# Optimization experiments

Hardware: AMD Instinct MI355X
Metric: run time of the kernel (lower is better)

The kernel has to match this reference:

```python
import jax, jax.numpy as jnp
import numpy as np


def setup_inputs() -> dict:
    key = jax.random.key(0)
    k1, k2 = jax.random.split(key)
    C, V, DEG = 256, 512, 6  # checks, variables, ~avg row degree (LDPC-sparse)
    H = (jax.random.uniform(k1, (C, V)) < DEG / V).astype(jnp.int32)
    llr = jax.random.normal(k2, (V,), dtype=jnp.float32) * 4.0  # LLR-scale values
    return {"llr": llr, "H": H, "max_iter": 2}


def reference(llr, H, max_iter):
    # Faithful translation of LDPCBeliefPropagation.forward, including its
    # sequential in-place update semantics (later node updates read earlier ones
    # within the same sweep).
    C, V = H.shape
    Hf = H.astype(jnp.float32)          # (C, V)
    Hb_T = (H == 1).T                   # (V, C) mask: Hb_T[v, j] = H[j, v]==1
    m_vtoc = jnp.ones((V, C), jnp.float32)
    m_ctov = jnp.zeros((C, V), jnp.float32)
    phi = lambda s: 2.0 * jnp.arctan(jnp.exp(0.5 * s))
    jidx = jnp.arange(V)

    for _ in range(max_iter):
        # --- variable->check pass: sequential over variable i ---
        # Original: m_vtoc[i, j] = sign(llr[i]) * prod_{v: H[j,v]==1} tanh(0.5*m_vtoc[v, j])
        # Step i writes row i; reads of column j see all rows < i already updated,
        # so we scan over i and recompute the masked column products each step.
        def p1(m, i):
            prod = jnp.prod(jnp.where(Hb_T, jnp.tanh(0.5 * m), 1.0), axis=0)  # (C,)
            return m.at[i].set(jnp.sign(llr[i]) * prod), None

        m_vtoc, _ = jax.lax.scan(p1, m_vtoc, jnp.arange(V))
        mv = m_vtoc

        # --- check->variable pass: sequential over check i ---
        # Original inner loop over j writes m_ctov[i, j] and reads column i of
        # m_ctov. Within fixed i, the only written element that is re-read is
        # (i, i) (written at j == i), so for j > i the sum gets the exact
        # correction H[i, j] * (v_new - old (i,i)). Bit-exact to the nested loop.
        def p2(m, i):
            col = m[:, i]                                  # (C,) old column i
            base = col @ Hf - mv[:, i]                     # (V,) masked sum - m_vtoc[j, i]
            v_new = phi(base[i])                           # value written at j == i
            adj = jnp.where(jidx > i, Hf[i] * (v_new - col[i]), 0.0)
            return m.at[i].set(phi(base + adj)), None

        m_ctov, _ = jax.lax.scan(p2, m_ctov, jnp.arange(C))

    soft = jnp.sign(llr) * jnp.prod(jnp.tanh(0.5 * m_ctov), axis=0)  # (V,)
    return jnp.where(soft > 0, 1, 0).astype(jnp.int32)[0:4]  # hardcoded [0:4] as in source
```

## Files before the change

### kernel.cpp

```cpp
#include <hip/hip_runtime.h>

#define CC 256
#define VV 512
#define MAXRD 26
#define MAXCD 18
#define PSTRIDE 27
#define RINGD 8
#define CLU 6

typedef __attribute__((address_space(1))) float gfloat;

__device__ __forceinline__ float sgnf(float x) {
    return (x > 0.f) ? 1.f : ((x < 0.f) ? -1.f : 0.f);
}
__device__ __forceinline__ float phi_f(float x) {
    return 2.0f * atanf(expf(0.5f * x));
}
__device__ __forceinline__ void lds_barrier() {
    asm volatile("s_waitcnt lgkmcnt(0)" ::: "memory");
    __builtin_amdgcn_sched_barrier(0);
    __builtin_amdgcn_s_barrier();
    __builtin_amdgcn_sched_barrier(0);
}

__global__ __launch_bounds__(256)
void ldpc_bp8(const float* __restrict__ llr_g, const int* __restrict__ H_g,
              const int* __restrict__ it_g, int* __restrict__ out_g,
              float* __restrict__ ws)
{
    __shared__ float              llr_s[VV];
    __shared__ unsigned int       rsign[CC];
    __shared__ unsigned int       rzero[CC];
    __shared__ unsigned short     rdeg_s[CC];
    __shared__ float              Pst[CC][PSTRIDE];
    __shared__ unsigned short     clistT[MAXCD][CC];
    __shared__ unsigned short     cdeg_s[CC];
    __shared__ float              colbuf[2][257];
    __shared__ float              ring[RINGD][CC];
    __shared__ unsigned long long rowmask[CC][4];
    __shared__ unsigned char      rowpre[CC][4];

    const int j  = threadIdx.x;
    const int wv = j >> 6, ln = j & 63;
    gfloat* __restrict__ mg = (gfloat*)ws;

    llr_s[j] = llr_g[j]; llr_s[j + CC] = llr_g[j + CC];
    __syncthreads();
    {   int d = 0; unsigned int sb = 0, zb = 0;
        const int4* hrow = (const int4*)(H_g + j * VV);
        for (int g = 0; g < VV / 4; ++g) {
            int4 h = hrow[g]; const int v = g * 4;
            if (h.x) { if (d < MAXRD) { float l = llr_s[v+0]; sb |= (l < 0.f) << d; zb |= (l == 0.f) << d; } ++d; }
            if (h.y) { if (d < MAXRD) { float l = llr_s[v+1]; sb |= (l < 0.f) << d; zb |= (l == 0.f) << d; } ++d; }
            if (h.z) { if (d < MAXRD) { float l = llr_s[v+2]; sb |= (l < 0.f) << d; zb |= (l == 0.f) << d; } ++d; }
            if (h.w) { if (d < MAXRD) { float l = llr_s[v+3]; sb |= (l < 0.f) << d; zb |= (l == 0.f) << d; } ++d; }
        }
        rdeg_s[j] = (unsigned short)(d < MAXRD ? d : MAXRD);
        rsign[j] = sb; rzero[j] = zb;
    }
    {   int d = 0;
        for (int c = 0; c < CC; ++c) {
            const int h = H_g[c * VV + j];
            const unsigned long long m = __ballot(h != 0);
            if (ln == 0) rowmask[c][wv] = m;
            if (h) { if (d < MAXCD) clistT[d][j] = (unsigned short)c; ++d; }
        }
        cdeg_s[j] = (unsigned short)(d < MAXCD ? d : MAXCD);
        for (int k = d; k < MAXCD; ++k) clistT[k][j] = 256;
    }
    colbuf[0][j] = 0.0f;
    if (j == 0) { colbuf[0][256] = 0.0f; colbuf[1][256] = 0.0f; }
    __syncthreads();
    {   const int p1 = __popcll(rowmask[j][0]);
        const int p2 = p1 + __popcll(rowmask[j][1]);
        const int p3 = p2 + __popcll(rowmask[j][2]);
        rowpre[j][0] = 0; rowpre[j][1] = (unsigned char)p1;
        rowpre[j][2] = (unsigned char)p2; rowpre[j][3] = (unsigned char)p3;
    }
    const int cl0 = clistT[0][j], cl1 = clistT[1][j], cl2 = clistT[2][j];
    const int cl3 = clistT[3][j], cl4 = clistT[4][j], cl5 = clistT[5][j];
    const int cd  = cdeg_s[j];
    __syncthreads();

    const int   max_iter = it_g[0];
    const int   total    = max_iter * CC;
    const float T05      = tanhf(0.5f);
    const float sgj      = sgnf(llr_s[j]);

    float sv_base = 0.f, sv_bi = 0.f, sv_cbs = 0.f;
    int   sv_hv = 0;
    float val_prev = 0.f, fprod = 1.0f;

    auto STEP = [&](int T, float& pf_issue, float& pf_use) {
        const int s  = T & 255;
        const int Tc = T + 1;
        const int X1 = Tc & 255;

        const float* cb = colbuf[T & 1];
        const float g0 = cb[cl0], g1 = cb[cl1], g2 = cb[cl2];
        const float g3 = cb[cl3], g4 = cb[cl4], g5 = cb[cl5];
        const unsigned long long rm = rowmask[s][wv];
        const int   p     = T - ((T - j) & 255);
        const float ringv = ring[p & (RINGD - 1)][X1];
        pf_issue = mg[((T + 4) & 255) * CC + j];

        if (T > 0) {
            float vnp;
            if (sv_hv) { float vnew = phi_f(sv_bi); vnp = phi_f(sv_base + (vnew - sv_cbs)); }
            else       vnp = phi_f(sv_base);
            val_prev = vnp;
            ring[(T - 1) & (RINGD - 1)][j] = vnp;
            mg[j * CC + ((T - 1) & 255)] = vnp;
            if (j < 4 && (T - 1) >= total - CC) fprod *= tanhf(0.5f * vnp);
        }

        if (s == 0) {
            const int pass = T >> 8;
            const int deg  = rdeg_s[j];
            const unsigned int sb = rsign[j], zb = rzero[j];
            float NP = 1.0f;
            for (int k = 0; k <= deg; ++k) {
                float P = NP;
                for (int idx = k; idx < deg; ++idx) {
                    float told;
                    if (pass == 0) told = T05;
                    else {
                        const float sg = ((zb >> idx) & 1u) ? 0.0f
                                       : (((sb >> idx) & 1u) ? -1.0f : 1.0f);
                        told = tanhf(0.5f * (sg * Pst[j][idx]));
                    }
                    P *= told;
                }
                Pst[j][k] = P;
                if (k < deg) {
                    const float sg = ((zb >> k) & 1u) ? 0.0f
                                   : (((sb >> k) & 1u) ? -1.0f : 1.0f);
                    NP *= tanhf(0.5f * (sg * P));
                }
            }
            lds_barrier();
        }

        if (Tc < total && p <= T - 2) {
            float v;
            if (p >= T - 8)    v = ringv;
            else if (p >= 0)   v = pf_use;
            else               v = 0.0f;
            colbuf[Tc & 1][j] = v;
        }

        const int  kj  = (int)rowpre[s][wv] + __popcll(rm & ((1ull << ln) - 1ull));
        const bool hit = (rm >> ln) & 1ull;
        float sum = 0.0f;
        sum += g0; sum += g1; sum += g2; sum += g3; sum += g4; sum += g5;
        for (int k = CLU; k < cd; ++k) sum += cb[clistT[k][j]];
        const float base = sum - sgj * Pst[s][kj];
        const bool hv = hit && (j > s);
        float bi = 0.f, cbs = 0.f;
        if (hv) {
            float bsum = 0.0f;
            bsum += cb[clistT[0][s]]; bsum += cb[clistT[1][s]];
            bsum += cb[clistT[2][s]]; bsum += cb[clistT[3][s]];
            bsum += cb[clistT[4][s]]; bsum += cb[clistT[5][s]];
            const int cds = cdeg_s[s];
            for (int k = CLU; k < cds; ++k) bsum += cb[clistT[k][s]];
            const int ki = (int)rowpre[s][s >> 6]
                         + __popcll(rowmask[s][s >> 6] & ((1ull << (s & 63)) - 1ull));
            bi  = bsum - sgnf(llr_s[s]) * Pst[s][ki];
            cbs = cb[s];
        }
        sv_base = base; sv_bi = bi; sv_cbs = cbs; sv_hv = hv ? 1 : 0;

        if (Tc < total && j == X1) {
            float vo;
            if (hv) { float vnew = phi_f(bi); vo = phi_f(base + (vnew - cbs)); }
            else    vo = phi_f(base);
            colbuf[Tc & 1][s] = vo;
            colbuf[Tc & 1][(T - 1) & 255] = val_prev;
        }

        lds_barrier();
    };

    float p0 = 0.f, p1r = 0.f, p2r = 0.f, p3r = 0.f;
    #pragma unroll 1
    for (int T4 = 0; T4 < total; T4 += 4) {
        STEP(T4 + 0, p0,  p1r);
        STEP(T4 + 1, p1r, p2r);
        STEP(T4 + 2, p2r, p3r);
        STEP(T4 + 3, p3r, p0);
    }

    {
        float vnp;
        if (sv_hv) { float vnew = phi_f(sv_bi); vnp = phi_f(sv_base + (vnew - sv_cbs)); }
        else       vnp = phi_f(sv_base);
        if (j < 4) {
            fprod *= tanhf(0.5f * vnp);
            const float soft = sgj * fprod;
            out_g[j] = (soft > 0.0f) ? 1 : 0;
        }
    }
}

extern "C" void kernel_launch(void* const* d_in, const int* in_sizes, int n_in,
                              void* d_out, int out_size, void* d_ws, size_t ws_size,
                              hipStream_t stream) {
    const float* llr = (const float*)d_in[0];
    const int*   H   = (const int*)d_in[1];
    const int*   mi  = (const int*)d_in[2];
    int*         out = (int*)d_out;
    float*       ws  = (float*)d_ws;
    hipLaunchKernelGGL(ldpc_bp8, dim3(1), dim3(256), 0, stream,
                       llr, H, mi, out, ws);
}
```

Before: 554.5 us.

## Process two check rows per barrier step with speculative diagonal value

Restructures the sequential check-to-variable sweep so each loop iteration handles two consecutive check rows (A and B) with one LDS barrier instead of two. Row B's dependency on row A's result is handled by having every thread recompute the single diagonal value that changes (dval) and substitute it wherever row s is referenced. The column buffers are doubled to hold two pending columns, and ring and prefetch logic is adapted. This aims to halve the barrier count on the serial critical path, at the cost of redundant per-thread arithmetic and more LDS reads per step.

```diff
diff --git a/kernel.cpp b/kernel.cpp
--- a/kernel.cpp
+++ b/kernel.cpp
@@ -5,7 +5,6 @@
 #define MAXRD 26
 #define MAXCD 18
 #define PSTRIDE 27
-#define RINGD 8
 #define CLU 6
 
 typedef __attribute__((address_space(1))) float gfloat;
@@ -24,7 +23,7 @@
 }
 
 __global__ __launch_bounds__(256)
-void ldpc_bp8(const float* __restrict__ llr_g, const int* __restrict__ H_g,
+void ldpc_bp9(const float* __restrict__ llr_g, const int* __restrict__ H_g,
               const int* __restrict__ it_g, int* __restrict__ out_g,
               float* __restrict__ ws)
 {
@@ -35,8 +34,8 @@
     __shared__ float              Pst[CC][PSTRIDE];
     __shared__ unsigned short     clistT[MAXCD][CC];
     __shared__ unsigned short     cdeg_s[CC];
-    __shared__ float              colbuf[2][257];
-    __shared__ float              ring[RINGD][CC];
+    __shared__ float              colbuf[2][2][257];
+    __shared__ float              ring[8][CC];
     __shared__ unsigned long long rowmask[CC][4];
     __shared__ unsigned char      rowpre[CC][4];
 
@@ -68,14 +67,19 @@
         cdeg_s[j] = (unsigned short)(d < MAXCD ? d : MAXCD);
         for (int k = d; k < MAXCD; ++k) clistT[k][j] = 256;
     }
-    colbuf[0][j] = 0.0f;
-    if (j == 0) { colbuf[0][256] = 0.0f; colbuf[1][256] = 0.0f; }
+    colbuf[0][0][j] = 0.f; colbuf[0][1][j] = 0.f;
+    colbuf[1][0][j] = 0.f; colbuf[1][1][j] = 0.f;
+    for (int r = 0; r < 8; ++r) ring[r][j] = 0.f;
+    if (j == 0) {
+        colbuf[0][0][256] = 0.f; colbuf[0][1][256] = 0.f;
+        colbuf[1][0][256] = 0.f; colbuf[1][1][256] = 0.f;
+    }
     __syncthreads();
-    {   const int p1 = __popcll(rowmask[j][0]);
-        const int p2 = p1 + __popcll(rowmask[j][1]);
-        const int p3 = p2 + __popcll(rowmask[j][2]);
-        rowpre[j][0] = 0; rowpre[j][1] = (unsigned char)p1;
-        rowpre[j][2] = (unsigned char)p2; rowpre[j][3] = (unsigned char)p3;
+    {   const int p1c = __popcll(rowmask[j][0]);
+        const int p2c = p1c + __popcll(rowmask[j][1]);
+        const int p3c = p2c + __popcll(rowmask[j][2]);
+        rowpre[j][0] = 0; rowpre[j][1] = (unsigned char)p1c;
+        rowpre[j][2] = (unsigned char)p2c; rowpre[j][3] = (unsigned char)p3c;
     }
     const int cl0 = clistT[0][j], cl1 = clistT[1][j], cl2 = clistT[2][j];
     const int cl3 = clistT[3][j], cl4 = clistT[4][j], cl5 = clistT[5][j];
@@ -87,35 +91,56 @@
     const float T05      = tanhf(0.5f);
     const float sgj      = sgnf(llr_s[j]);
 
-    float sv_base = 0.f, sv_bi = 0.f, sv_cbs = 0.f;
-    int   sv_hv = 0;
-    float val_prev = 0.f, fprod = 1.0f;
-
-    auto STEP = [&](int T, float& pf_issue, float& pf_use) {
-        const int s  = T & 255;
-        const int Tc = T + 1;
-        const int X1 = Tc & 255;
-
-        const float* cb = colbuf[T & 1];
-        const float g0 = cb[cl0], g1 = cb[cl1], g2 = cb[cl2];
-        const float g3 = cb[cl3], g4 = cb[cl4], g5 = cb[cl5];
-        const unsigned long long rm = rowmask[s][wv];
-        const int   p     = T - ((T - j) & 255);
-        const float ringv = ring[p & (RINGD - 1)][X1];
-        pf_issue = mg[((T + 4) & 255) * CC + j];
-
-        if (T > 0) {
-            float vnp;
-            if (sv_hv) { float vnew = phi_f(sv_bi); vnp = phi_f(sv_base + (vnew - sv_cbs)); }
-            else       vnp = phi_f(sv_base);
-            val_prev = vnp;
-            ring[(T - 1) & (RINGD - 1)][j] = vnp;
-            mg[j * CC + ((T - 1) & 255)] = vnp;
-            if (j < 4 && (T - 1) >= total - CC) fprod *= tanhf(0.5f * vnp);
+    float svA_base = 0.f, svA_bi = 0.f, svA_cbs = 0.f; int svA_hv = 0;
+    float svB_base = 0.f, svB_bi = 0.f, svB_cbs = 0.f; int svB_hv = 0;
+    float pfu0 = 0.f, pfu1 = 0.f;
+    float fprod = 1.0f;
+
+    #pragma unroll 1
+    for (int Ts = 0; Ts < total; Ts += 2) {
+        const int s   = Ts & 255;
+        const int X1v = s + 1;
+        const int X2v = (Ts + 2) & 255;
+        const int X3v = (Ts + 3) & 255;
+        const int pr  = (Ts >> 1) & 1;
+        const float* cbA = colbuf[pr][0];
+        const float* cbB = colbuf[pr][1];
+        float* nxA = colbuf[pr ^ 1][0];
+        float* nxB = colbuf[pr ^ 1][1];
+
+        const float gA0 = cbA[cl0], gA1 = cbA[cl1], gA2 = cbA[cl2];
+        const float gA3 = cbA[cl3], gA4 = cbA[cl4], gA5 = cbA[cl5];
+        const float gB0 = cbB[cl0], gB1 = cbB[cl1], gB2 = cbB[cl2];
+        const float gB3 = cbB[cl3], gB4 = cbB[cl4], gB5 = cbB[cl5];
+        const unsigned long long rmA = rowmask[s][wv];
+        const unsigned long long rmB = rowmask[X1v][wv];
+        const int p = (Ts + 1) - ((Ts + 1 - j) & 255);
+        const float ringvA = ring[p & 7][X2v];
+        const float ringvB = ring[p & 7][X3v];
+        const float pfi0 = mg[((Ts + 4) & 255) * CC + j];
+        const float pfi1 = mg[((Ts + 5) & 255) * CC + j];
+        const int dc0 = clistT[0][X1v], dc1 = clistT[1][X1v], dc2 = clistT[2][X1v];
+        const int dc3 = clistT[3][X1v], dc4 = clistT[4][X1v], dc5 = clistT[5][X1v];
+        const int cdd = cdeg_s[X1v];
+
+        float vnpA = 0.f, vnpB = 0.f;
+        if (Ts >= 2) {
+            if (svA_hv) { float vn = phi_f(svA_bi); vnpA = phi_f(svA_base + (vn - svA_cbs)); }
+            else        vnpA = phi_f(svA_base);
+            if (svB_hv) { float vn = phi_f(svB_bi); vnpB = phi_f(svB_base + (vn - svB_cbs)); }
+            else        vnpB = phi_f(svB_base);
+            ring[(Ts - 2) & 7][j] = vnpA;
+            ring[(Ts - 1) & 7][j] = vnpB;
+            mg[j * CC + ((Ts - 2) & 255)] = vnpA;
+            mg[j * CC + ((Ts - 1) & 255)] = vnpB;
+            if (j < 4) {
+                if (Ts - 2 >= total - CC) fprod *= tanhf(0.5f * vnpA);
+                if (Ts - 1 >= total - CC) fprod *= tanhf(0.5f * vnpB);
+            }
         }
 
         if (s == 0) {
-            const int pass = T >> 8;
+            const int pass = Ts >> 8;
             const int deg  = rdeg_s[j];
             const unsigned int sb = rsign[j], zb = rzero[j];
             float NP = 1.0f;
@@ -141,62 +166,114 @@
             lds_barrier();
         }
 
-        if (Tc < total && p <= T - 2) {
-            float v;
-            if (p >= T - 8)    v = ringv;
-            else if (p >= 0)   v = pf_use;
-            else               v = 0.0f;
-            colbuf[Tc & 1][j] = v;
-        }
-
-        const int  kj  = (int)rowpre[s][wv] + __popcll(rm & ((1ull << ln) - 1ull));
-        const bool hit = (rm >> ln) & 1ull;
-        float sum = 0.0f;
-        sum += g0; sum += g1; sum += g2; sum += g3; sum += g4; sum += g5;
-        for (int k = CLU; k < cd; ++k) sum += cb[clistT[k][j]];
-        const float base = sum - sgj * Pst[s][kj];
-        const bool hv = hit && (j > s);
-        float bi = 0.f, cbs = 0.f;
-        if (hv) {
+        float dsum = 0.0f;
+        dsum += cbA[dc0]; dsum += cbA[dc1]; dsum += cbA[dc2];
+        dsum += cbA[dc3]; dsum += cbA[dc4]; dsum += cbA[dc5];
+        for (int k = CLU; k < cdd; ++k) dsum += cbA[clistT[k][X1v]];
+        const int kjd = (int)rowpre[s][X1v >> 6]
+                      + __popcll(rowmask[s][X1v >> 6] & ((1ull << (X1v & 63)) - 1ull));
+        const float bX1 = dsum - sgnf(llr_s[X1v]) * Pst[s][kjd];
+        const bool diag_hit = (rowmask[s][X1v >> 6] >> (X1v & 63)) & 1ull;
+        float dval;
+        if (diag_hit) {
+            float bs_ = 0.0f;
+            const int cds = cdeg_s[s];
+            for (int k = 0; k < cds; ++k) bs_ += cbA[clistT[k][s]];
+            const int kis = (int)rowpre[s][s >> 6]
+                          + __popcll(rowmask[s][s >> 6] & ((1ull << (s & 63)) - 1ull));
+            const float bis = bs_ - sgnf(llr_s[s]) * Pst[s][kis];
+            dval = phi_f(bX1 + (phi_f(bis) - cbA[s]));
+        } else {
+            dval = phi_f(bX1);
+        }
+
+        const unsigned long long lanelt = (1ull << ln) - 1ull;
+        const int  kjA  = (int)rowpre[s][wv] + __popcll(rmA & lanelt);
+        const bool hitA = (rmA >> ln) & 1ull;
+        float sumA = 0.0f;
+        sumA += gA0; sumA += gA1; sumA += gA2; sumA += gA3; sumA += gA4; sumA += gA5;
+        for (int k = CLU; k < cd; ++k) sumA += cbA[clistT[k][j]];
+        const float baseA = sumA - sgj * Pst[s][kjA];
+        const bool hvA = hitA && (j > s);
+        float biA = 0.f, cbsA = 0.f;
+        if (hvA) {
             float bsum = 0.0f;
-            bsum += cb[clistT[0][s]]; bsum += cb[clistT[1][s]];
-            bsum += cb[clistT[2][s]]; bsum += cb[clistT[3][s]];
-            bsum += cb[clistT[4][s]]; bsum += cb[clistT[5][s]];
             const int cds = cdeg_s[s];
-            for (int k = CLU; k < cds; ++k) bsum += cb[clistT[k][s]];
-            const int ki = (int)rowpre[s][s >> 6]
-                         + __popcll(rowmask[s][s >> 6] & ((1ull << (s & 63)) - 1ull));
-            bi  = bsum - sgnf(llr_s[s]) * Pst[s][ki];
-            cbs = cb[s];
-        }
-        sv_base = base; sv_bi = bi; sv_cbs = cbs; sv_hv = hv ? 1 : 0;
-
-        if (Tc < total && j == X1) {
-            float vo;
-            if (hv) { float vnew = phi_f(bi); vo = phi_f(base + (vnew - cbs)); }
-            else    vo = phi_f(base);
-            colbuf[Tc & 1][s] = vo;
-            colbuf[Tc & 1][(T - 1) & 255] = val_prev;
-        }
+            for (int k = 0; k < cds; ++k) bsum += cbA[clistT[k][s]];
+            const int kis2 = (int)rowpre[s][s >> 6]
+                           + __popcll(rowmask[s][s >> 6] & ((1ull << (s & 63)) - 1ull));
+            biA  = bsum - sgnf(llr_s[s]) * Pst[s][kis2];
+            cbsA = cbA[s];
+        }
+
+        const int  kjB  = (int)rowpre[X1v][wv] + __popcll(rmB & lanelt);
+        const bool hitB = (rmB >> ln) & 1ull;
+        const float tB0 = (cl0 == s) ? dval : gB0;
+        const float tB1 = (cl1 == s) ? dval : gB1;
+        const float tB2 = (cl2 == s) ? dval : gB2;
+        const float tB3 = (cl3 == s) ? dval : gB3;
+        const float tB4 = (cl4 == s) ? dval : gB4;
+        const float tB5 = (cl5 == s) ? dval : gB5;
+        float sumB = 0.0f;
+        sumB += tB0; sumB += tB1; sumB += tB2; sumB += tB3; sumB += tB4; sumB += tB5;
+        for (int k = CLU; k < cd; ++k) {
+            const int ci = clistT[k][j];
+            sumB += (ci == s) ? dval : cbB[ci];
+        }
+        const float baseB = sumB - sgj * Pst[X1v][kjB];
+        const bool hvB = hitB && (j > X1v);
+        float biB = 0.f, cbsB = 0.f;
+        if (hvB) {
+            float bsum = 0.0f;
+            const int cdsB = cdeg_s[X1v];
+            for (int k = 0; k < cdsB; ++k) {
+                const int ci = clistT[k][X1v];
+                bsum += (ci == s) ? dval : cbB[ci];
+            }
+            const int kiB = (int)rowpre[X1v][X1v >> 6]
+                          + __popcll(rowmask[X1v][X1v >> 6] & ((1ull << (X1v & 63)) - 1ull));
+            biB  = bsum - sgnf(llr_s[X1v]) * Pst[X1v][kiB];
+            cbsB = cbB[X1v];
+        }
+
+        if (j == X2v || j == X3v) {
+            float voT, voT1;
+            if (hvA) voT  = phi_f(baseA + (phi_f(biA) - cbsA)); else voT  = phi_f(baseA);
+            if (hvB) voT1 = phi_f(baseB + (phi_f(biB) - cbsB)); else voT1 = phi_f(baseB);
+            float* nx = (j == X2v) ? nxA : nxB;
+            nx[s]   = voT;
+            nx[X1v] = voT1;
+            if (Ts >= 2) {
+                nx[(Ts - 1) & 255] = vnpB;
+                nx[(Ts - 2) & 255] = vnpA;
+            }
+        }
+
+        if (p <= Ts - 3) {
+            float vA, vB;
+            if (p < 0)           { vA = 0.0f;   vB = 0.0f;   }
+            else if (p >= Ts - 8){ vA = ringvA; vB = ringvB; }
+            else                 { vA = pfu0;   vB = pfu1;   }
+            nxA[j] = vA;
+            nxB[j] = vB;
+        }
+
+        svA_base = baseA; svA_bi = biA; svA_cbs = cbsA; svA_hv = hvA ? 1 : 0;
+        svB_base = baseB; svB_bi = biB; svB_cbs = cbsB; svB_hv = hvB ? 1 : 0;
+        pfu0 = pfi0; pfu1 = pfi1;
 
         lds_barrier();
-    };
-
-    float p0 = 0.f, p1r = 0.f, p2r = 0.f, p3r = 0.f;
-    #pragma unroll 1
-    for (int T4 = 0; T4 < total; T4 += 4) {
-        STEP(T4 + 0, p0,  p1r);
-        STEP(T4 + 1, p1r, p2r);
-        STEP(T4 + 2, p2r, p3r);
-        STEP(T4 + 3, p3r, p0);
     }
 
     {
-        float vnp;
-        if (sv_hv) { float vnew = phi_f(sv_bi); vnp = phi_f(sv_base + (vnew - sv_cbs)); }
-        else       vnp = phi_f(sv_base);
+        float vnpA, vnpB;
+        if (svA_hv) { float vn = phi_f(svA_bi); vnpA = phi_f(svA_base + (vn - svA_cbs)); }
+        else        vnpA = phi_f(svA_base);
+        if (svB_hv) { float vn = phi_f(svB_bi); vnpB = phi_f(svB_base + (vn - svB_cbs)); }
+        else        vnpB = phi_f(svB_base);
         if (j < 4) {
-            fprod *= tanhf(0.5f * vnp);
+            fprod *= tanhf(0.5f * vnpA);
+            fprod *= tanhf(0.5f * vnpB);
             const float soft = sgj * fprod;
             out_g[j] = (soft > 0.0f) ? 1 : 0;
         }
@@ -211,6 +288,6 @@
     const int*   mi  = (const int*)d_in[2];
     int*         out = (int*)d_out;
     float*       ws  = (float*)d_ws;
-    hipLaunchKernelGGL(ldpc_bp8, dim3(1), dim3(256), 0, stream,
+    hipLaunchKernelGGL(ldpc_bp9, dim3(1), dim3(256), 0, stream,
                        llr, H, mi, out, ws);
 }
```

New measurement: 682.2 us. +23.0%, slower.

## Halve block to 128 threads with two columns per thread to cheapen barriers

Applied to the files above, without the earlier changes.

Launches the single-block kernel with 128 threads instead of 256, so each thread handles two variable columns j and j+128. The sequential per-step loop then synchronises 2 wavefronts per barrier instead of 4, which should make the 512 barrier-bound steps cheaper. In exchange each thread does twice the LDS reads and phi evaluations per step, and the shared bsum computation is done once for both columns. It also zero-initialises the ring buffer.

```diff
diff --git a/kernel.cpp b/kernel.cpp
--- a/kernel.cpp
+++ b/kernel.cpp
@@ -5,8 +5,8 @@
 #define MAXRD 26
 #define MAXCD 18
 #define PSTRIDE 27
-#define RINGD 8
 #define CLU 6
+#define NT  128
 
 typedef __attribute__((address_space(1))) float gfloat;
 
@@ -23,10 +23,10 @@
     __builtin_amdgcn_sched_barrier(0);
 }
 
-__global__ __launch_bounds__(256)
-void ldpc_bp8(const float* __restrict__ llr_g, const int* __restrict__ H_g,
-              const int* __restrict__ it_g, int* __restrict__ out_g,
-              float* __restrict__ ws)
+__global__ __launch_bounds__(NT)
+void ldpc_bp10(const float* __restrict__ llr_g, const int* __restrict__ H_g,
+               const int* __restrict__ it_g, int* __restrict__ out_g,
+               float* __restrict__ ws)
 {
     __shared__ float              llr_s[VV];
     __shared__ unsigned int       rsign[CC];
@@ -36,18 +36,25 @@
     __shared__ unsigned short     clistT[MAXCD][CC];
     __shared__ unsigned short     cdeg_s[CC];
     __shared__ float              colbuf[2][257];
-    __shared__ float              ring[RINGD][CC];
+    __shared__ float              ring[8][CC];
     __shared__ unsigned long long rowmask[CC][4];
     __shared__ unsigned char      rowpre[CC][4];
 
-    const int j  = threadIdx.x;
-    const int wv = j >> 6, ln = j & 63;
+    const int tid = threadIdx.x;
+    const int j0  = tid, j1 = tid + NT;
+    const int wv  = tid >> 6, ln = tid & 63;
     gfloat* __restrict__ mg = (gfloat*)ws;
 
-    llr_s[j] = llr_g[j]; llr_s[j + CC] = llr_g[j + CC];
+    llr_s[tid]       = llr_g[tid];
+    llr_s[tid + 128] = llr_g[tid + 128];
+    llr_s[tid + 256] = llr_g[tid + 256];
+    llr_s[tid + 384] = llr_g[tid + 384];
     __syncthreads();
-    {   int d = 0; unsigned int sb = 0, zb = 0;
-        const int4* hrow = (const int4*)(H_g + j * VV);
+    #pragma unroll 1
+    for (int rr = 0; rr < 2; ++rr) {
+        const int c = tid + rr * NT;
+        int d = 0; unsigned int sb = 0, zb = 0;
+        const int4* hrow = (const int4*)(H_g + c * VV);
         for (int g = 0; g < VV / 4; ++g) {
             int4 h = hrow[g]; const int v = g * 4;
             if (h.x) { if (d < MAXRD) { float l = llr_s[v+0]; sb |= (l < 0.f) << d; zb |= (l == 0.f) << d; } ++d; }
@@ -55,150 +62,205 @@
             if (h.z) { if (d < MAXRD) { float l = llr_s[v+2]; sb |= (l < 0.f) << d; zb |= (l == 0.f) << d; } ++d; }
             if (h.w) { if (d < MAXRD) { float l = llr_s[v+3]; sb |= (l < 0.f) << d; zb |= (l == 0.f) << d; } ++d; }
         }
-        rdeg_s[j] = (unsigned short)(d < MAXRD ? d : MAXRD);
-        rsign[j] = sb; rzero[j] = zb;
-    }
-    {   int d = 0;
+        rdeg_s[c] = (unsigned short)(d < MAXRD ? d : MAXRD);
+        rsign[c] = sb; rzero[c] = zb;
+    }
+    {
+        int d0 = 0, d1 = 0;
         for (int c = 0; c < CC; ++c) {
-            const int h = H_g[c * VV + j];
-            const unsigned long long m = __ballot(h != 0);
-            if (ln == 0) rowmask[c][wv] = m;
-            if (h) { if (d < MAXCD) clistT[d][j] = (unsigned short)c; ++d; }
-        }
-        cdeg_s[j] = (unsigned short)(d < MAXCD ? d : MAXCD);
-        for (int k = d; k < MAXCD; ++k) clistT[k][j] = 256;
-    }
-    colbuf[0][j] = 0.0f;
-    if (j == 0) { colbuf[0][256] = 0.0f; colbuf[1][256] = 0.0f; }
+            const int h0 = H_g[c * VV + j0];
+            const int h1 = H_g[c * VV + j1];
+            const unsigned long long m0 = __ballot(h0 != 0);
+            const unsigned long long m1 = __ballot(h1 != 0);
+            if (ln == 0) { rowmask[c][wv] = m0; rowmask[c][2 + wv] = m1; }
+            if (h0) { if (d0 < MAXCD) clistT[d0][j0] = (unsigned short)c; ++d0; }
+            if (h1) { if (d1 < MAXCD) clistT[d1][j1] = (unsigned short)c; ++d1; }
+        }
+        cdeg_s[j0] = (unsigned short)(d0 < MAXCD ? d0 : MAXCD);
+        cdeg_s[j1] = (unsigned short)(d1 < MAXCD ? d1 : MAXCD);
+        for (int k = d0; k < MAXCD; ++k) clistT[k][j0] = 256;
+        for (int k = d1; k < MAXCD; ++k) clistT[k][j1] = 256;
+    }
+    colbuf[0][j0] = 0.0f; colbuf[0][j1] = 0.0f;
+    #pragma unroll
+    for (int r = 0; r < 8; ++r) { ring[r][j0] = 0.0f; ring[r][j1] = 0.0f; }
+    if (tid == 0) { colbuf[0][256] = 0.0f; colbuf[1][256] = 0.0f; }
     __syncthreads();
-    {   const int p1 = __popcll(rowmask[j][0]);
-        const int p2 = p1 + __popcll(rowmask[j][1]);
-        const int p3 = p2 + __popcll(rowmask[j][2]);
-        rowpre[j][0] = 0; rowpre[j][1] = (unsigned char)p1;
-        rowpre[j][2] = (unsigned char)p2; rowpre[j][3] = (unsigned char)p3;
-    }
-    const int cl0 = clistT[0][j], cl1 = clistT[1][j], cl2 = clistT[2][j];
-    const int cl3 = clistT[3][j], cl4 = clistT[4][j], cl5 = clistT[5][j];
-    const int cd  = cdeg_s[j];
+    #pragma unroll 1
+    for (int rr = 0; rr < 2; ++rr) {
+        const int c = tid + rr * NT;
+        const int q1 = __popcll(rowmask[c][0]);
+        const int q2 = q1 + __popcll(rowmask[c][1]);
+        const int q3 = q2 + __popcll(rowmask[c][2]);
+        rowpre[c][0] = 0; rowpre[c][1] = (unsigned char)q1;
+        rowpre[c][2] = (unsigned char)q2; rowpre[c][3] = (unsigned char)q3;
+    }
+    const int c00 = clistT[0][j0], c01 = clistT[1][j0], c02 = clistT[2][j0];
+    const int c03 = clistT[3][j0], c04 = clistT[4][j0], c05 = clistT[5][j0];
+    const int c10 = clistT[0][j1], c11 = clistT[1][j1], c12 = clistT[2][j1];
+    const int c13 = clistT[3][j1], c14 = clistT[4][j1], c15 = clistT[5][j1];
+    const int cd0 = cdeg_s[j0], cd1 = cdeg_s[j1];
     __syncthreads();
 
     const int   max_iter = it_g[0];
     const int   total    = max_iter * CC;
     const float T05      = tanhf(0.5f);
-    const float sgj      = sgnf(llr_s[j]);
-
-    float sv_base = 0.f, sv_bi = 0.f, sv_cbs = 0.f;
-    int   sv_hv = 0;
-    float val_prev = 0.f, fprod = 1.0f;
-
-    auto STEP = [&](int T, float& pf_issue, float& pf_use) {
+    const float sg0      = sgnf(llr_s[j0]);
+    const float sg1      = sgnf(llr_s[j1]);
+
+    float sv0_base = 0.f, sv0_bi = 0.f, sv0_cbs = 0.f; int sv0_hv = 0;
+    float sv1_base = 0.f, sv1_bi = 0.f, sv1_cbs = 0.f; int sv1_hv = 0;
+    float vp0 = 0.f, vp1 = 0.f;
+    float fprod = 1.0f;
+
+    auto STEP = [&](int T, float& pia, float& pib, float& pua, float& pub) {
         const int s  = T & 255;
         const int Tc = T + 1;
         const int X1 = Tc & 255;
 
         const float* cb = colbuf[T & 1];
-        const float g0 = cb[cl0], g1 = cb[cl1], g2 = cb[cl2];
-        const float g3 = cb[cl3], g4 = cb[cl4], g5 = cb[cl5];
-        const unsigned long long rm = rowmask[s][wv];
-        const int   p     = T - ((T - j) & 255);
-        const float ringv = ring[p & (RINGD - 1)][X1];
-        pf_issue = mg[((T + 4) & 255) * CC + j];
+        const float a0 = cb[c00], a1 = cb[c01], a2 = cb[c02];
+        const float a3 = cb[c03], a4 = cb[c04], a5 = cb[c05];
+        const float b0 = cb[c10], b1 = cb[c11], b2 = cb[c12];
+        const float b3 = cb[c13], b4 = cb[c14], b5 = cb[c15];
+        const unsigned long long rm0 = rowmask[s][wv];
+        const unsigned long long rm1 = rowmask[s][2 + wv];
+        const int p0  = T - ((T - j0) & 255);
+        const int p1v = T - ((T - j1) & 255);
+        const float ringv0 = ring[p0 & 7][X1];
+        const float ringv1 = ring[p1v & 7][X1];
+        pia = mg[((T + 4) & 255) * CC + j0];
+        pib = mg[((T + 4) & 255) * CC + j1];
 
         if (T > 0) {
-            float vnp;
-            if (sv_hv) { float vnew = phi_f(sv_bi); vnp = phi_f(sv_base + (vnew - sv_cbs)); }
-            else       vnp = phi_f(sv_base);
-            val_prev = vnp;
-            ring[(T - 1) & (RINGD - 1)][j] = vnp;
-            mg[j * CC + ((T - 1) & 255)] = vnp;
-            if (j < 4 && (T - 1) >= total - CC) fprod *= tanhf(0.5f * vnp);
+            float v0, v1;
+            if (sv0_hv) { float vn = phi_f(sv0_bi); v0 = phi_f(sv0_base + (vn - sv0_cbs)); }
+            else        v0 = phi_f(sv0_base);
+            if (sv1_hv) { float vn = phi_f(sv1_bi); v1 = phi_f(sv1_base + (vn - sv1_cbs)); }
+            else        v1 = phi_f(sv1_base);
+            vp0 = v0; vp1 = v1;
+            ring[(T - 1) & 7][j0] = v0;
+            ring[(T - 1) & 7][j1] = v1;
+            mg[j0 * CC + ((T - 1) & 255)] = v0;
+            mg[j1 * CC + ((T - 1) & 255)] = v1;
+            if (tid < 4 && (T - 1) >= total - CC) fprod *= tanhf(0.5f * v0);
         }
 
         if (s == 0) {
             const int pass = T >> 8;
-            const int deg  = rdeg_s[j];
-            const unsigned int sb = rsign[j], zb = rzero[j];
-            float NP = 1.0f;
-            for (int k = 0; k <= deg; ++k) {
-                float P = NP;
-                for (int idx = k; idx < deg; ++idx) {
-                    float told;
-                    if (pass == 0) told = T05;
-                    else {
-                        const float sg = ((zb >> idx) & 1u) ? 0.0f
-                                       : (((sb >> idx) & 1u) ? -1.0f : 1.0f);
-                        told = tanhf(0.5f * (sg * Pst[j][idx]));
+            #pragma unroll 1
+            for (int rr = 0; rr < 2; ++rr) {
+                const int c   = tid + rr * NT;
+                const int deg = rdeg_s[c];
+                const unsigned int sb = rsign[c], zb = rzero[c];
+                float NP = 1.0f;
+                for (int k = 0; k <= deg; ++k) {
+                    float P = NP;
+                    for (int idx = k; idx < deg; ++idx) {
+                        float told;
+                        if (pass == 0) told = T05;
+                        else {
+                            const float sg = ((zb >> idx) & 1u) ? 0.0f
+                                           : (((sb >> idx) & 1u) ? -1.0f : 1.0f);
+                            told = tanhf(0.5f * (sg * Pst[c][idx]));
+                        }
+                        P *= told;
                     }
-                    P *= told;
-                }
-                Pst[j][k] = P;
-                if (k < deg) {
-                    const float sg = ((zb >> k) & 1u) ? 0.0f
-                                   : (((sb >> k) & 1u) ? -1.0f : 1.0f);
-                    NP *= tanhf(0.5f * (sg * P));
+                    Pst[c][k] = P;
+                    if (k < deg) {
+                        const float sg = ((zb >> k) & 1u) ? 0.0f
+                                       : (((sb >> k) & 1u) ? -1.0f : 1.0f);
+                        NP *= tanhf(0.5f * (sg * P));
+                    }
                 }
             }
             lds_barrier();
         }
 
-        if (Tc < total && p <= T - 2) {
-            float v;
-            if (p >= T - 8)    v = ringv;
-            else if (p >= 0)   v = pf_use;
-            else               v = 0.0f;
-            colbuf[Tc & 1][j] = v;
-        }
-
-        const int  kj  = (int)rowpre[s][wv] + __popcll(rm & ((1ull << ln) - 1ull));
-        const bool hit = (rm >> ln) & 1ull;
-        float sum = 0.0f;
-        sum += g0; sum += g1; sum += g2; sum += g3; sum += g4; sum += g5;
-        for (int k = CLU; k < cd; ++k) sum += cb[clistT[k][j]];
-        const float base = sum - sgj * Pst[s][kj];
-        const bool hv = hit && (j > s);
-        float bi = 0.f, cbs = 0.f;
-        if (hv) {
+        if (Tc < total) {
+            if (p0 <= T - 2) {
+                float v;
+                if (p0 < 0)           v = 0.0f;
+                else if (p0 >= T - 8) v = ringv0;
+                else                  v = pua;
+                colbuf[Tc & 1][j0] = v;
+            }
+            if (p1v <= T - 2) {
+                float v;
+                if (p1v < 0)           v = 0.0f;
+                else if (p1v >= T - 8) v = ringv1;
+                else                   v = pub;
+                colbuf[Tc & 1][j1] = v;
+            }
+        }
+
+        const unsigned long long lanelt = (1ull << ln) - 1ull;
+        const int  kj0  = (int)rowpre[s][wv] + __popcll(rm0 & lanelt);
+        const bool hit0 = (rm0 >> ln) & 1ull;
+        float sum0 = 0.0f;
+        sum0 += a0; sum0 += a1; sum0 += a2; sum0 += a3; sum0 += a4; sum0 += a5;
+        for (int k = CLU; k < cd0; ++k) sum0 += cb[clistT[k][j0]];
+        const float base0 = sum0 - sg0 * Pst[s][kj0];
+        const bool hv0 = hit0 && (j0 > s);
+
+        const int  kj1  = (int)rowpre[s][2 + wv] + __popcll(rm1 & lanelt);
+        const bool hit1 = (rm1 >> ln) & 1ull;
+        float sum1 = 0.0f;
+        sum1 += b0; sum1 += b1; sum1 += b2; sum1 += b3; sum1 += b4; sum1 += b5;
+        for (int k = CLU; k < cd1; ++k) sum1 += cb[clistT[k][j1]];
+        const float base1 = sum1 - sg1 * Pst[s][kj1];
+        const bool hv1 = hit1 && (j1 > s);
+
+        float bi0 = 0.f, cbs0 = 0.f, bi1 = 0.f, cbs1 = 0.f;
+        if (hv0 | hv1) {
             float bsum = 0.0f;
-            bsum += cb[clistT[0][s]]; bsum += cb[clistT[1][s]];
-            bsum += cb[clistT[2][s]]; bsum += cb[clistT[3][s]];
-            bsum += cb[clistT[4][s]]; bsum += cb[clistT[5][s]];
             const int cds = cdeg_s[s];
-            for (int k = CLU; k < cds; ++k) bsum += cb[clistT[k][s]];
-            const int ki = (int)rowpre[s][s >> 6]
-                         + __popcll(rowmask[s][s >> 6] & ((1ull << (s & 63)) - 1ull));
-            bi  = bsum - sgnf(llr_s[s]) * Pst[s][ki];
-            cbs = cb[s];
-        }
-        sv_base = base; sv_bi = bi; sv_cbs = cbs; sv_hv = hv ? 1 : 0;
-
-        if (Tc < total && j == X1) {
+            for (int k = 0; k < cds; ++k) bsum += cb[clistT[k][s]];
+            const int kis = (int)rowpre[s][s >> 6]
+                          + __popcll(rowmask[s][s >> 6] & ((1ull << (s & 63)) - 1ull));
+            const float biv = bsum - sgnf(llr_s[s]) * Pst[s][kis];
+            const float cbv = cb[s];
+            if (hv0) { bi0 = biv; cbs0 = cbv; }
+            if (hv1) { bi1 = biv; cbs1 = cbv; }
+        }
+
+        if (Tc < total && (j0 == X1 || j1 == X1)) {
+            const bool  own0 = (j0 == X1);
+            const float ob   = own0 ? base0 : base1;
+            const bool  ohv  = own0 ? hv0 : hv1;
+            const float obi  = own0 ? bi0 : bi1;
+            const float ocb  = own0 ? cbs0 : cbs1;
             float vo;
-            if (hv) { float vnew = phi_f(bi); vo = phi_f(base + (vnew - cbs)); }
-            else    vo = phi_f(base);
+            if (ohv) { float vn = phi_f(obi); vo = phi_f(ob + (vn - ocb)); }
+            else     vo = phi_f(ob);
             colbuf[Tc & 1][s] = vo;
-            colbuf[Tc & 1][(T - 1) & 255] = val_prev;
-        }
+            colbuf[Tc & 1][(T - 1) & 255] = own0 ? vp0 : vp1;
+        }
+
+        sv0_base = base0; sv0_bi = bi0; sv0_cbs = cbs0; sv0_hv = hv0 ? 1 : 0;
+        sv1_base = base1; sv1_bi = bi1; sv1_cbs = cbs1; sv1_hv = hv1 ? 1 : 0;
 
         lds_barrier();
     };
 
-    float p0 = 0.f, p1r = 0.f, p2r = 0.f, p3r = 0.f;
+    float q0a = 0.f, q0b = 0.f, q1a = 0.f, q1b = 0.f;
+    float q2a = 0.f, q2b = 0.f, q3a = 0.f, q3b = 0.f;
     #pragma unroll 1
     for (int T4 = 0; T4 < total; T4 += 4) {
-        STEP(T4 + 0, p0,  p1r);
-        STEP(T4 + 1, p1r, p2r);
-        STEP(T4 + 2, p2r, p3r);
-        STEP(T4 + 3, p3r, p0);
+        STEP(T4 + 0, q0a, q0b, q1a, q1b);
+        STEP(T4 + 1, q1a, q1b, q2a, q2b);
+        STEP(T4 + 2, q2a, q2b, q3a, q3b);
+        STEP(T4 + 3, q3a, q3b, q0a, q0b);
     }
 
     {
-        float vnp;
-        if (sv_hv) { float vnew = phi_f(sv_bi); vnp = phi_f(sv_base + (vnew - sv_cbs)); }
-        else       vnp = phi_f(sv_base);
-        if (j < 4) {
-            fprod *= tanhf(0.5f * vnp);
-            const float soft = sgj * fprod;
-            out_g[j] = (soft > 0.0f) ? 1 : 0;
+        float v0;
+        if (sv0_hv) { float vn = phi_f(sv0_bi); v0 = phi_f(sv0_base + (vn - sv0_cbs)); }
+        else        v0 = phi_f(sv0_base);
+        if (tid < 4) {
+            fprod *= tanhf(0.5f * v0);
+            const float soft = sg0 * fprod;
+            out_g[tid] = (soft > 0.0f) ? 1 : 0;
         }
     }
 }
@@ -211,6 +273,6 @@
     const int*   mi  = (const int*)d_in[2];
     int*         out = (int*)d_out;
     float*       ws  = (float*)d_ws;
-    hipLaunchKernelGGL(ldpc_bp8, dim3(1), dim3(256), 0, stream,
+    hipLaunchKernelGGL(ldpc_bp10, dim3(1), dim3(NT), 0, stream,
                        llr, H, mi, out, ws);
 }
```

After: 906.2 us. 1.63x slower.
